# Kernel tuning notes

Measured on AMD Instinct MI355X. Metric: run time of the kernel, lower is better.

## Reference

```python
import jax, jax.numpy as jnp
import numpy as np

N = 131072          # total nodes
E = 4194304         # edges (avg degree 32)
SUB = 16            # size_subgraph_samples
HID = 256


def _gcn_norm(src, dst, n):
    # add self-loops
    loops = jnp.arange(n, dtype=src.dtype)
    src = jnp.concatenate([src, loops])
    dst = jnp.concatenate([dst, loops])
    deg = jax.ops.segment_sum(jnp.ones_like(dst, dtype=jnp.float32), dst, num_segments=n)
    dinv = jnp.where(deg > 0, jax.lax.rsqrt(deg), 0.0)
    norm = dinv[src] * dinv[dst]  # [E+N]
    return src, dst, norm


def _gcn_conv(x, W, b, src, dst, norm, n):
    h = x @ W                                  # [N, out]
    msg = h[src] * norm[:, None]               # gather + scale
    agg = jax.ops.segment_sum(msg, dst, num_segments=n)
    return agg + b


def setup_inputs() -> dict:
    key = jax.random.key(0)
    ks = jax.random.split(key, 6)
    x = jax.random.normal(ks[0], (N, 128), dtype=jnp.float32)
    edge_index = jax.random.randint(ks[1], (2, E), 0, N, dtype=jnp.int64)
    W1 = jax.random.normal(ks[2], (128, HID), dtype=jnp.float32) * (1.0 / np.sqrt(128))
    b1 = jnp.zeros((HID,), dtype=jnp.float32)
    W2 = jax.random.normal(ks[3], (HID, HID), dtype=jnp.float32) * (1.0 / np.sqrt(HID))
    b2 = jnp.zeros((HID,), dtype=jnp.float32)
    Wout = jax.random.normal(ks[4], (HID * SUB, 1), dtype=jnp.float32) * (1.0 / np.sqrt(HID * SUB))
    bout = jnp.zeros((1,), dtype=jnp.float32)
    return {"x": x, "edge_index": edge_index, "W1": W1, "b1": b1,
            "W2": W2, "b2": b2, "Wout": Wout, "bout": bout}


def reference(x, edge_index, W1, b1, W2, b2, Wout, bout):
    n = x.shape[0]
    src, dst, norm = _gcn_norm(edge_index[0], edge_index[1], n)
    h = jax.nn.relu(_gcn_conv(x, W1, b1, src, dst, norm, n))
    h = jax.nn.relu(_gcn_conv(h, W2, b2, src, dst, norm, n))
    h = h.reshape(n // SUB, SUB * h.shape[1])   # [8192, 4096]
    return h @ Wout + bout                       # [8192, 1]
```

## Files before the change

kernel.cpp:

```cpp
#include <hip/hip_runtime.h>
#include <stdint.h>

#define NN 131072
#define NE 4194304
#define BKT 256
#define BKT_SH 9
#define BCAP 20480

typedef __bf16 bf16x8 __attribute__((ext_vector_type(8)));
typedef float  floatx4 __attribute__((ext_vector_type(4)));
typedef unsigned short u16x8 __attribute__((ext_vector_type(8)));

__device__ __forceinline__ float bf2f(unsigned short u) {
  union { unsigned int i; float f; } v; v.i = ((unsigned int)u) << 16; return v.f;
}
__device__ __forceinline__ unsigned short f2bf(float f) {
  union { float f; unsigned int i; } v; v.f = f;
  unsigned int r = v.i + 0x7fffu + ((v.i >> 16) & 1u);
  return (unsigned short)(r >> 16);
}


__global__ __launch_bounds__(256) void k_bzero(int* __restrict__ bktCnt) {
  bktCnt[threadIdx.x] = 0;
}

__global__ __launch_bounds__(1024) void k_bucket(const int* __restrict__ src,
                                                 const int* __restrict__ dst,
                                                 int* __restrict__ bktCnt,
                                                 unsigned int* __restrict__ bktBuf) {
  __shared__ int hist[BKT];
  __shared__ int base[BKT];
  const int t = threadIdx.x;
  if (t < BKT) hist[t] = 0;
  __syncthreads();
  const int e0 = (blockIdx.x * 1024 + t);
  const int4 s = ((const int4*)src)[e0];
  const int4 d = ((const int4*)dst)[e0];
  const int b0 = ((unsigned)d.x) >> BKT_SH, b1 = ((unsigned)d.y) >> BKT_SH;
  const int b2 = ((unsigned)d.z) >> BKT_SH, b3 = ((unsigned)d.w) >> BKT_SH;
  const int r0 = atomicAdd(&hist[b0], 1);
  const int r1 = atomicAdd(&hist[b1], 1);
  const int r2 = atomicAdd(&hist[b2], 1);
  const int r3 = atomicAdd(&hist[b3], 1);
  __syncthreads();
  if (t < BKT) base[t] = atomicAdd(&bktCnt[t], hist[t]);
  __syncthreads();
  const unsigned p0 = (((unsigned)s.x) << BKT_SH) | (d.x & 511);
  const unsigned p1 = (((unsigned)s.y) << BKT_SH) | (d.y & 511);
  const unsigned p2 = (((unsigned)s.z) << BKT_SH) | (d.z & 511);
  const unsigned p3 = (((unsigned)s.w) << BKT_SH) | (d.w & 511);
  bktBuf[(size_t)b0 * BCAP + base[b0] + r0] = p0;
  bktBuf[(size_t)b1 * BCAP + base[b1] + r1] = p1;
  bktBuf[(size_t)b2 * BCAP + base[b2] + r2] = p2;
  bktBuf[(size_t)b3 * BCAP + base[b3] + r3] = p3;
}

__global__ __launch_bounds__(1024) void k_csr(const int* __restrict__ bktCnt,
                                              const unsigned int* __restrict__ bktBuf,
                                              int* __restrict__ row_ptr,
                                              float* __restrict__ dinv,
                                              int* __restrict__ csr) {
  __shared__ int bsum[BKT];
  __shared__ int histA[512];
  __shared__ int histB[512];
  __shared__ int sc[512];
  __shared__ int curA[512];
  __shared__ int curB[512];
  const int b = blockIdx.x;
  const int t = threadIdx.x;
  const int rep = t & 1;
  if (t < BKT) bsum[t] = bktCnt[t];
  if (t < 512) { histA[t] = 0; histB[t] = 0; }
  __syncthreads();
  for (int off = 1; off < BKT; off <<= 1) {
    int v = 0;
    if (t < BKT && t >= off) v = bsum[t - off];
    __syncthreads();
    if (t < BKT) bsum[t] += v;
    __syncthreads();
  }
  const int sz = bktCnt[b];
  const int csrBase = bsum[b] - sz;
  const unsigned int* eb = bktBuf + (size_t)b * BCAP;
  for (int i = t; i < sz; i += 1024)
    atomicAdd(rep ? &histB[eb[i] & 511] : &histA[eb[i] & 511], 1);
  __syncthreads();
  if (t < 512) sc[t] = histA[t] + histB[t];
  __syncthreads();
  for (int off = 1; off < 512; off <<= 1) {
    int v = 0;
    if (t < 512 && t >= off) v = sc[t - off];
    __syncthreads();
    if (t < 512) sc[t] += v;
    __syncthreads();
  }
  if (t < 512) {
    const int cnt = histA[t] + histB[t];
    const int ex = csrBase + sc[t] - cnt;
    row_ptr[b * 512 + t] = ex;
    curA[t] = ex;
    curB[t] = ex + histA[t];
    dinv[b * 512 + t] = rsqrtf((float)(cnt + 1));
  }
  if (b == BKT - 1 && t == 0) row_ptr[NN] = NE;
  __syncthreads();
  for (int i = t; i < sz; i += 1024) {
    const unsigned e = eb[i];
    const int n = e & 511;
    const int pos = atomicAdd(rep ? &curB[n] : &curA[n], 1);
    csr[pos] = (int)(e >> BKT_SH);
  }
}

__global__ __launch_bounds__(256) void k_cvt(const float* __restrict__ X,
                                             unsigned short* __restrict__ Xb) {
  const int t = blockIdx.x * 256 + threadIdx.x;
  const float4 v = ((const float4*)X)[t];
  ushort4 o;
  o.x = f2bf(v.x); o.y = f2bf(v.y); o.z = f2bf(v.z); o.w = f2bf(v.w);
  ((ushort4*)Xb)[t] = o;
}

__global__ __launch_bounds__(256) void k_swizzle2(const float* __restrict__ W1,
                                                  unsigned short* __restrict__ Wsw1,
                                                  const float* __restrict__ W2,
                                                  unsigned short* __restrict__ Wsw2) {
  int b = blockIdx.x;
  const float* W; unsigned short* Wsw;
  if (b < 128) { W = W1; Wsw = Wsw1; } else { W = W2; Wsw = Wsw2; b -= 128; }
  const int t = b * 256 + threadIdx.x;
  const int k = t >> 8, n = t & 255;
  const int s = ((k >> 5) * 16 + (n >> 4)) * 512 + ((k >> 3) & 3) * 128 + (n & 15) * 8 + (k & 7);
  Wsw[s] = f2bf(W[t]);
}

__global__ __launch_bounds__(256) void agg_h(const unsigned short* __restrict__ X,
                                             const int* __restrict__ row_ptr,
                                             const int* __restrict__ csr,
                                             const float* __restrict__ dinv,
                                             unsigned short* __restrict__ Y,
                                             int F, int foff, int node_base) {
  const int lane = threadIdx.x & 63;
  const int node = node_base + ((blockIdx.x * blockDim.x + threadIdx.x) >> 6);
  const int sub = lane >> 4;
  const int fl = lane & 15;
  const int start = row_ptr[node];
  const int end = row_ptr[node + 1];
  const float di = dinv[node];
  float a[8] = {0.f, 0.f, 0.f, 0.f, 0.f, 0.f, 0.f, 0.f};
  const unsigned short* Xf = X + foff + fl * 8;

  for (int e = start; e < end; e += 64) {
    const int nload = min(end - e, 64);
    int s_l = node;
    float w_l = 0.0f;
    if (lane < nload) {
      s_l = __builtin_nontemporal_load(&csr[e + lane]);
      w_l = dinv[s_l];
    }
    for (int j = 0; j < nload; j += 16) {
      const int i0 = j + sub, i1 = j + 4 + sub, i2 = j + 8 + sub, i3 = j + 12 + sub;
      const int s0 = __shfl(s_l, i0); const float w0 = __shfl(w_l, i0);
      const int s1 = __shfl(s_l, i1); const float w1 = __shfl(w_l, i1);
      const int s2 = __shfl(s_l, i2); const float w2 = __shfl(w_l, i2);
      const int s3 = __shfl(s_l, i3); const float w3 = __shfl(w_l, i3);
      const u16x8 r0 = *(const u16x8*)(Xf + (size_t)s0 * F);
      const u16x8 r1 = *(const u16x8*)(Xf + (size_t)s1 * F);
      const u16x8 r2 = *(const u16x8*)(Xf + (size_t)s2 * F);
      const u16x8 r3 = *(const u16x8*)(Xf + (size_t)s3 * F);
#pragma unroll
      for (int i = 0; i < 8; ++i) a[i] = fmaf(w0, bf2f(r0[i]), a[i]);
#pragma unroll
      for (int i = 0; i < 8; ++i) a[i] = fmaf(w1, bf2f(r1[i]), a[i]);
#pragma unroll
      for (int i = 0; i < 8; ++i) a[i] = fmaf(w2, bf2f(r2[i]), a[i]);
#pragma unroll
      for (int i = 0; i < 8; ++i) a[i] = fmaf(w3, bf2f(r3[i]), a[i]);
    }
  }
#pragma unroll
  for (int i = 0; i < 8; ++i) a[i] += __shfl_xor(a[i], 16);
#pragma unroll
  for (int i = 0; i < 8; ++i) a[i] += __shfl_xor(a[i], 32);
  const u16x8 sv = *(const u16x8*)(Xf + (size_t)node * F);
#pragma unroll
  for (int i = 0; i < 8; ++i) a[i] = fmaf(di, bf2f(sv[i]), a[i]);
  if (sub == 0) {
    u16x8 o;
#pragma unroll
    for (int i = 0; i < 8; ++i) o[i] = f2bf(di * a[i]);
    *(u16x8*)(Y + (size_t)node * F + foff + fl * 8) = o;
  }
}

template <int K>
__global__ __launch_bounds__(512) void k_gemm(const unsigned short* __restrict__ A,
                                              const unsigned short* __restrict__ Wsw,
                                              const float* __restrict__ bias,
                                              unsigned short* __restrict__ out) {
  __shared__ unsigned short lW[128 * 256];
  const int tid = threadIdx.x;
  const int wave = tid >> 6;
  const int lane = tid & 63;
  const int q = lane >> 4;
  const int m16 = lane & 15;
  const size_t baseM = (size_t)blockIdx.x * 256;

  floatx4 acc[2][16];
#pragma unroll
  for (int t = 0; t < 2; ++t)
#pragma unroll
    for (int nt = 0; nt < 16; ++nt) acc[t][nt] = (floatx4){0.f, 0.f, 0.f, 0.f};

  const size_t rowA0 = baseM + wave * 32 + m16;
  const size_t rowA1 = rowA0 + 16;

  for (int half = 0; half < K / 128; ++half) {
    __syncthreads();
    const uint4* gsrc = (const uint4*)(Wsw + half * 32768);
    uint4* ldst = (uint4*)lW;
#pragma unroll
    for (int i = 0; i < 8; ++i) ldst[i * 512 + tid] = gsrc[i * 512 + tid];
    __syncthreads();

#pragma unroll
    for (int kc = 0; kc < 4; ++kc) {
      const int koff = half * 128 + kc * 32 + q * 8;
      const bf16x8 av0 = *(const bf16x8*)(A + rowA0 * K + koff);
      const bf16x8 av1 = *(const bf16x8*)(A + rowA1 * K + koff);
#pragma unroll
      for (int nt = 0; nt < 16; ++nt) {
        const bf16x8 bv = *(const bf16x8*)(&lW[(kc * 16 + nt) * 512 + lane * 8]);
        acc[0][nt] = __builtin_amdgcn_mfma_f32_16x16x32_bf16(av0, bv, acc[0][nt], 0, 0, 0);
        acc[1][nt] = __builtin_amdgcn_mfma_f32_16x16x32_bf16(av1, bv, acc[1][nt], 0, 0, 0);
      }
    }
  }
  const int rq = (lane >> 4) * 4;
#pragma unroll
  for (int t = 0; t < 2; ++t) {
#pragma unroll
    for (int nt = 0; nt < 16; ++nt) {
      const int col = nt * 16 + m16;
      const float bv = bias[col];
#pragma unroll
      for (int r = 0; r < 4; ++r) {
        const size_t row = baseM + wave * 32 + t * 16 + rq + r;
        float v = acc[t][nt][r] + bv;
        v = fmaxf(v, 0.0f);
        out[row * 256 + col] = f2bf(v);
      }
    }
  }
}

__global__ __launch_bounds__(512) void k_gemm_out(const unsigned short* __restrict__ A,
                                                  const unsigned short* __restrict__ Wsw,
                                                  const float* __restrict__ bias,
                                                  const float* __restrict__ Wout,
                                                  const float* __restrict__ bout,
                                                  float* __restrict__ out) {
  constexpr int K = 256;
  __shared__ unsigned short lW[128 * 256];
  const int tid = threadIdx.x;
  const int wave = tid >> 6;
  const int lane = tid & 63;
  const int q = lane >> 4;
  const int m16 = lane & 15;
  const size_t baseM = (size_t)blockIdx.x * 256;

  floatx4 acc[2][16];
#pragma unroll
  for (int t = 0; t < 2; ++t)
#pragma unroll
    for (int nt = 0; nt < 16; ++nt) acc[t][nt] = (floatx4){0.f, 0.f, 0.f, 0.f};

  const size_t rowA0 = baseM + wave * 32 + m16;
  const size_t rowA1 = rowA0 + 16;

  for (int half = 0; half < 2; ++half) {
    __syncthreads();
    const uint4* gsrc = (const uint4*)(Wsw + half * 32768);
    uint4* ldst = (uint4*)lW;
#pragma unroll
    for (int i = 0; i < 8; ++i) ldst[i * 512 + tid] = gsrc[i * 512 + tid];
    __syncthreads();

#pragma unroll
    for (int kc = 0; kc < 4; ++kc) {
      const int koff = half * 128 + kc * 32 + q * 8;
      const bf16x8 av0 = *(const bf16x8*)(A + rowA0 * K + koff);
      const bf16x8 av1 = *(const bf16x8*)(A + rowA1 * K + koff);
#pragma unroll
      for (int nt = 0; nt < 16; ++nt) {
        const bf16x8 bv = *(const bf16x8*)(&lW[(kc * 16 + nt) * 512 + lane * 8]);
        acc[0][nt] = __builtin_amdgcn_mfma_f32_16x16x32_bf16(av0, bv, acc[0][nt], 0, 0, 0);
        acc[1][nt] = __builtin_amdgcn_mfma_f32_16x16x32_bf16(av1, bv, acc[1][nt], 0, 0, 0);
      }
    }
  }
  const int rq = (lane >> 4) * 4;
  float p0 = 0.f, p1 = 0.f;
#pragma unroll
  for (int nt = 0; nt < 16; ++nt) {
    const int col = nt * 16 + m16;
    const float bv = bias[col];
#pragma unroll
    for (int r = 0; r < 4; ++r) {
      const float wv = Wout[(rq + r) * 256 + col];
      const float v0 = fmaxf(acc[0][nt][r] + bv, 0.0f);
      const float v1 = fmaxf(acc[1][nt][r] + bv, 0.0f);
      p0 = fmaf(v0, wv, p0);
      p1 = fmaf(v1, wv, p1);
    }
  }
#pragma unroll
  for (int off = 32; off > 0; off >>= 1) {
    p0 += __shfl_xor(p0, off);
    p1 += __shfl_xor(p1, off);
  }
  if (lane == 0) {
    const float bo = bout[0];
    const int g = blockIdx.x * 16 + wave * 2;
    out[g]     = p0 + bo;
    out[g + 1] = p1 + bo;
  }
}

extern "C" void kernel_launch(void* const* d_in, const int* in_sizes, int n_in,
                              void* d_out, int out_size, void* d_ws, size_t ws_size,
                              hipStream_t stream) {
  const float* x    = (const float*)d_in[0];
  const int*   ei   = (const int*)d_in[1];
  const float* W1   = (const float*)d_in[2];
  const float* b1   = (const float*)d_in[3];
  const float* W2   = (const float*)d_in[4];
  const float* b2   = (const float*)d_in[5];
  const float* Wout = (const float*)d_in[6];
  const float* bout = (const float*)d_in[7];
  float* out = (float*)d_out;

  char* ws = (char*)d_ws;
  size_t off = 0;
  auto alloc = [&](size_t bytes) {
    char* p = ws + off;
    off += (bytes + 511) & ~(size_t)511;
    return p;
  };
  int*            row_ptr = (int*)alloc(((size_t)NN + 1) * 4);
  float*          dinv    = (float*)alloc((size_t)NN * 4);
  int*            bktCnt  = (int*)alloc(BKT * 4);
  unsigned int*   bktBuf  = (unsigned int*)alloc((size_t)BKT * BCAP * 4);
  int*            csr     = (int*)alloc((size_t)NE * 4);
  unsigned short* Wsw1    = (unsigned short*)alloc(128 * 256 * 2);
  unsigned short* Wsw2    = (unsigned short*)alloc(256 * 256 * 2);
  unsigned short* xb      = (unsigned short*)alloc((size_t)NN * 128 * 2);
  unsigned short* bufA    = (unsigned short*)alloc((size_t)NN * 256 * 2);
  unsigned short* bufB    = (unsigned short*)alloc((size_t)NN * 256 * 2);
  (void)in_sizes; (void)n_in; (void)out_size; (void)ws_size;

  const int* src = ei;
  const int* dst = ei + NE;

  hipLaunchKernelGGL(k_bzero,  dim3(1), dim3(256), 0, stream, bktCnt);
  hipLaunchKernelGGL(k_bucket, dim3(NE / 4096), dim3(1024), 0, stream, src, dst, bktCnt, bktBuf);
  hipLaunchKernelGGL(k_csr,    dim3(BKT), dim3(1024), 0, stream, bktCnt, bktBuf, row_ptr, dinv, csr);
  hipLaunchKernelGGL(k_cvt,    dim3(NN * 128 / 4 / 256), dim3(256), 0, stream, x, xb);
  hipLaunchKernelGGL(k_swizzle2, dim3(384), dim3(256), 0, stream, W1, Wsw1, W2, Wsw2);

  hipLaunchKernelGGL(agg_h, dim3(NN / 8), dim3(256), 0, stream, xb, row_ptr, csr, dinv, bufA, 128, 0, 0);
  hipLaunchKernelGGL(agg_h, dim3(NN / 8), dim3(256), 0, stream, xb, row_ptr, csr, dinv, bufA, 128, 0, NN / 2);
  hipLaunchKernelGGL(k_gemm<128>, dim3(NN / 256), dim3(512), 0, stream, bufA, Wsw1, b1, bufB);
  hipLaunchKernelGGL(agg_h, dim3(NN / 8), dim3(256), 0, stream, bufB, row_ptr, csr, dinv, bufA, 256, 0, 0);
  hipLaunchKernelGGL(agg_h, dim3(NN / 8), dim3(256), 0, stream, bufB, row_ptr, csr, dinv, bufA, 256, 0, NN / 2);
  hipLaunchKernelGGL(agg_h, dim3(NN / 8), dim3(256), 0, stream, bufB, row_ptr, csr, dinv, bufA, 256, 128, 0);
  hipLaunchKernelGGL(agg_h, dim3(NN / 8), dim3(256), 0, stream, bufB, row_ptr, csr, dinv, bufA, 256, 128, NN / 2);
  hipLaunchKernelGGL(k_gemm_out, dim3(NN / 256), dim3(512), 0, stream, bufA, Wsw2, b2, Wout, bout, out);
}
```

Baseline: 731.9 us.

## Stage bucketed edges in LDS for coalesced writes and merge node-half launches

The bucketing kernel now does a block-local prefix scan over bucket counts and stages packed edges in shared memory sorted by bucket. Each bucket's run is then written to global memory contiguously, instead of four scattered stores per thread. Separately, the aggregation kernels that were split into two node halves are merged into single full-range launches, which removes launch overhead. The cost is extra shared memory (about 20 KB) and eight extra barriers for the scan, which may reduce occupancy of the bucket kernel.

Result: faster. 705.1 us (-3.7%).

```diff
diff --git a/kernel.cpp b/kernel.cpp
--- a/kernel.cpp
+++ b/kernel.cpp
@@ -30,11 +30,14 @@
                                                  int* __restrict__ bktCnt,
                                                  unsigned int* __restrict__ bktBuf) {
   __shared__ int hist[BKT];
-  __shared__ int base[BKT];
+  __shared__ int lofs[BKT];
+  __shared__ int gbase[BKT];
+  __shared__ unsigned int ebuf[4096];
+  __shared__ unsigned char bkt[4096];
   const int t = threadIdx.x;
   if (t < BKT) hist[t] = 0;
   __syncthreads();
-  const int e0 = (blockIdx.x * 1024 + t);
+  const int e0 = blockIdx.x * 1024 + t;
   const int4 s = ((const int4*)src)[e0];
   const int4 d = ((const int4*)dst)[e0];
   const int b0 = ((unsigned)d.x) >> BKT_SH, b1 = ((unsigned)d.y) >> BKT_SH;
@@ -44,16 +47,32 @@
   const int r2 = atomicAdd(&hist[b2], 1);
   const int r3 = atomicAdd(&hist[b3], 1);
   __syncthreads();
-  if (t < BKT) base[t] = atomicAdd(&bktCnt[t], hist[t]);
-  __syncthreads();
-  const unsigned p0 = (((unsigned)s.x) << BKT_SH) | (d.x & 511);
-  const unsigned p1 = (((unsigned)s.y) << BKT_SH) | (d.y & 511);
-  const unsigned p2 = (((unsigned)s.z) << BKT_SH) | (d.z & 511);
-  const unsigned p3 = (((unsigned)s.w) << BKT_SH) | (d.w & 511);
-  bktBuf[(size_t)b0 * BCAP + base[b0] + r0] = p0;
-  bktBuf[(size_t)b1 * BCAP + base[b1] + r1] = p1;
-  bktBuf[(size_t)b2 * BCAP + base[b2] + r2] = p2;
-  bktBuf[(size_t)b3 * BCAP + base[b3] + r3] = p3;
+  if (t < BKT) lofs[t] = hist[t];
+  __syncthreads();
+  for (int off = 1; off < BKT; off <<= 1) {
+    int v = 0;
+    if (t < BKT && t >= off) v = lofs[t - off];
+    __syncthreads();
+    if (t < BKT) lofs[t] += v;
+    __syncthreads();
+  }
+  {
+    const int s0i = lofs[b0] - hist[b0] + r0;
+    const int s1i = lofs[b1] - hist[b1] + r1;
+    const int s2i = lofs[b2] - hist[b2] + r2;
+    const int s3i = lofs[b3] - hist[b3] + r3;
+    ebuf[s0i] = (((unsigned)s.x) << BKT_SH) | (d.x & 511); bkt[s0i] = (unsigned char)b0;
+    ebuf[s1i] = (((unsigned)s.y) << BKT_SH) | (d.y & 511); bkt[s1i] = (unsigned char)b1;
+    ebuf[s2i] = (((unsigned)s.z) << BKT_SH) | (d.z & 511); bkt[s2i] = (unsigned char)b2;
+    ebuf[s3i] = (((unsigned)s.w) << BKT_SH) | (d.w & 511); bkt[s3i] = (unsigned char)b3;
+  }
+  if (t < BKT)
+    gbase[t] = atomicAdd(&bktCnt[t], hist[t]) - (lofs[t] - hist[t]);
+  __syncthreads();
+  for (int i = t; i < 4096; i += 1024) {
+    const int bb = bkt[i];
+    bktBuf[(size_t)bb * BCAP + gbase[bb] + i] = ebuf[i];
+  }
 }
 
 __global__ __launch_bounds__(1024) void k_csr(const int* __restrict__ bktCnt,
@@ -140,9 +159,9 @@
                                              const int* __restrict__ csr,
                                              const float* __restrict__ dinv,
                                              unsigned short* __restrict__ Y,
-                                             int F, int foff, int node_base) {
+                                             int F, int foff) {
   const int lane = threadIdx.x & 63;
-  const int node = node_base + ((blockIdx.x * blockDim.x + threadIdx.x) >> 6);
+  const int node = (blockIdx.x * blockDim.x + threadIdx.x) >> 6;
   const int sub = lane >> 4;
   const int fl = lane & 15;
   const int start = row_ptr[node];
@@ -369,12 +388,9 @@
   hipLaunchKernelGGL(k_cvt,    dim3(NN * 128 / 4 / 256), dim3(256), 0, stream, x, xb);
   hipLaunchKernelGGL(k_swizzle2, dim3(384), dim3(256), 0, stream, W1, Wsw1, W2, Wsw2);
 
-  hipLaunchKernelGGL(agg_h, dim3(NN / 8), dim3(256), 0, stream, xb, row_ptr, csr, dinv, bufA, 128, 0, 0);
-  hipLaunchKernelGGL(agg_h, dim3(NN / 8), dim3(256), 0, stream, xb, row_ptr, csr, dinv, bufA, 128, 0, NN / 2);
+  hipLaunchKernelGGL(agg_h, dim3(NN / 4), dim3(256), 0, stream, xb, row_ptr, csr, dinv, bufA, 128, 0);
   hipLaunchKernelGGL(k_gemm<128>, dim3(NN / 256), dim3(512), 0, stream, bufA, Wsw1, b1, bufB);
-  hipLaunchKernelGGL(agg_h, dim3(NN / 8), dim3(256), 0, stream, bufB, row_ptr, csr, dinv, bufA, 256, 0, 0);
-  hipLaunchKernelGGL(agg_h, dim3(NN / 8), dim3(256), 0, stream, bufB, row_ptr, csr, dinv, bufA, 256, 0, NN / 2);
-  hipLaunchKernelGGL(agg_h, dim3(NN / 8), dim3(256), 0, stream, bufB, row_ptr, csr, dinv, bufA, 256, 128, 0);
-  hipLaunchKernelGGL(agg_h, dim3(NN / 8), dim3(256), 0, stream, bufB, row_ptr, csr, dinv, bufA, 256, 128, NN / 2);
+  hipLaunchKernelGGL(agg_h, dim3(NN / 4), dim3(256), 0, stream, bufB, row_ptr, csr, dinv, bufA, 256, 0);
+  hipLaunchKernelGGL(agg_h, dim3(NN / 4), dim3(256), 0, stream, bufB, row_ptr, csr, dinv, bufA, 256, 128);
   hipLaunchKernelGGL(k_gemm_out, dim3(NN / 256), dim3(512), 0, stream, bufA, Wsw2, b2, Wout, bout, out);
 }
```
